# Performance work log

Measured on AMD Instinct MI355X. Metric: run time of the kernel, lower is better.

Reference implementation:

```python
import jax, jax.numpy as jnp
import numpy as np

N_NODES = 25000
N_EDGES = 400000
HIDDEN = 256
NUM_FILTERS = 256
NUM_GAUSSIANS = 50
CUTOFF = 10.0


def ssp(x):
    # ShiftedSoftplus: softplus(x) - log(2)
    return jax.nn.softplus(x) - jnp.log(2.0).astype(x.dtype)


def setup_inputs() -> dict:
    key = jax.random.key(0)
    ks = jax.random.split(key, 12)
    s = 0.05
    return {
        "h": jax.random.normal(ks[0], (N_NODES, HIDDEN), dtype=jnp.float32),
        "pos": jax.random.uniform(ks[1], (N_NODES, 3), dtype=jnp.float32) * CUTOFF,
        "lin1_w": jax.random.normal(ks[2], (HIDDEN, NUM_FILTERS), dtype=jnp.float32) * s,
        "lin2_w": jax.random.normal(ks[3], (NUM_FILTERS, HIDDEN), dtype=jnp.float32) * s,
        "lin2_b": jnp.zeros((HIDDEN,), dtype=jnp.float32),
        "mlp_w1": jax.random.normal(ks[4], (NUM_GAUSSIANS, NUM_FILTERS), dtype=jnp.float32) * s,
        "mlp_b1": jnp.zeros((NUM_FILTERS,), dtype=jnp.float32),
        "mlp_w2": jax.random.normal(ks[5], (NUM_FILTERS, NUM_FILTERS), dtype=jnp.float32) * s,
        "mlp_b2": jnp.zeros((NUM_FILTERS,), dtype=jnp.float32),
        "lin_w": jax.random.normal(ks[6], (HIDDEN, HIDDEN), dtype=jnp.float32) * s,
        "lin_b": jnp.zeros((HIDDEN,), dtype=jnp.float32),
        "edge_index": jax.random.randint(ks[7], (2, N_EDGES), 0, N_NODES, dtype=jnp.int32),
    }


def reference(h, pos, lin1_w, lin2_w, lin2_b, mlp_w1, mlp_b1, mlp_w2, mlp_b2,
              lin_w, lin_b, edge_index):
    row, col = edge_index[0], edge_index[1]  # source, target (PyG convention)

    # edge distances
    diff = pos[row] - pos[col]                       # [E, 3]
    edge_weight = jnp.linalg.norm(diff, axis=-1)     # [E]

    # GaussianSmearing(0, cutoff, num_gaussians)
    offset = jnp.linspace(0.0, CUTOFF, NUM_GAUSSIANS, dtype=h.dtype)
    coeff = -0.5 / (offset[1] - offset[0]) ** 2
    edge_attr = jnp.exp(coeff * (edge_weight[:, None] - offset) ** 2)  # [E, G]

    # CFConv filter network * cosine cutoff
    W = ssp(edge_attr @ mlp_w1 + mlp_b1) @ mlp_w2 + mlp_b2             # [E, F]
    C = 0.5 * (jnp.cos(edge_weight * (jnp.pi / CUTOFF)) + 1.0)         # [E]
    W = W * C[:, None]

    # gather - multiply - scatter-add
    x = h @ lin1_w                                                     # [N, F] (no bias)
    msg = x[row] * W                                                   # [E, F]
    agg = jax.ops.segment_sum(msg, col, num_segments=N_NODES)          # [N, F]

    x = agg @ lin2_w + lin2_b
    x = ssp(x)
    h_update = x @ lin_w + lin_b                                       # [N, H]
    return (h_update, pos)
```

## Files before the change

kernel.cpp:

```cpp
#include <hip/hip_runtime.h>
#include <hip/hip_bf16.h>

#define N_NODES 25000
#define N_EDGES 400000
#define NTILES (N_EDGES / 32)

typedef __attribute__((ext_vector_type(8))) __bf16 bf16x8;
typedef __attribute__((ext_vector_type(4))) float f32x4;
typedef __attribute__((ext_vector_type(2))) unsigned uint32x2;

#define BAR() do {                                          \
    asm volatile("s_waitcnt lgkmcnt(0)" ::: "memory");      \
    __builtin_amdgcn_s_barrier();                           \
    asm volatile("" ::: "memory");                          \
} while (0)

static __device__ __forceinline__ unsigned short bfbits(float f) {
    __bf16 h = (__bf16)f;
    return __builtin_bit_cast(unsigned short, h);
}
static __device__ __forceinline__ float bf2f(unsigned short u) {
    return __builtin_bit_cast(float, ((unsigned)u) << 16);
}
static __device__ __forceinline__ float ssp_f(float x) {
    const float t = __builtin_amdgcn_exp2f(x * 1.44269504f);
    return 0.69314718f * (__builtin_amdgcn_logf(1.f + t) - 1.f);
}

template<int EPI, int OBF, int ABF>
__global__ __launch_bounds__(256, 2)
void node_gemm(const void* __restrict__ Av, const float* __restrict__ B,
               const float* __restrict__ bias, void* __restrict__ outv, int M)
{
    extern __shared__ char lds[];
    const int tid  = threadIdx.x;
    const int half = blockIdx.x & 1;
    const int jblk = half << 7;
    const int row0 = (blockIdx.x >> 1) << 7;

    {
        const int j   = tid & 127;
        const int k2b = (tid >> 7) << 6;
        for (int i = 0; i < 64; ++i) {
            const int k = (k2b + i) * 2;
            const float b0 = B[k * 256 + jblk + j];
            const float b1 = B[(k + 1) * 256 + jblk + j];
            const unsigned pack = (unsigned)bfbits(b0) | ((unsigned)bfbits(b1) << 16);
            *(unsigned*)(lds + ((j * 512 + k * 2) ^ ((j & 7) << 4))) = pack;
        }
    }
    __syncthreads();

    const int wave = tid >> 6;
    const int l    = tid & 63;
    const int lrow = l & 15;
    const int kg   = (l >> 4) << 3;

    f32x4 acc[8][2];
    const f32x4 z4 = {0.f, 0.f, 0.f, 0.f};
    #pragma unroll
    for (int m = 0; m < 8; ++m) { acc[m][0] = z4; acc[m][1] = z4; }

    #pragma unroll
    for (int ks = 0; ks < 8; ++ks) {
        const int k0 = (ks << 5) + kg;
        bf16x8 bfr[2];
        #pragma unroll
        for (int n = 0; n < 2; ++n) {
            const int jl = (wave << 5) + (n << 4) + lrow;
            bfr[n] = *(const bf16x8*)(lds + ((jl * 512 + k0 * 2) ^ ((jl & 7) << 4)));
        }
        #pragma unroll
        for (int m = 0; m < 8; ++m) {
            const int row = row0 + (m << 4) + lrow;
            bf16x8 af;
            if (row < M) {
                if (ABF) {
                    af = *(const bf16x8*)((const __bf16*)Av + row * 256 + k0);
                } else {
                    const float* ap = (const float*)Av + row * 256 + k0;
                    const f32x4 a0 = *(const f32x4*)(ap);
                    const f32x4 a1 = *(const f32x4*)(ap + 4);
                    #pragma unroll
                    for (int b = 0; b < 4; ++b) { af[b] = (__bf16)a0[b]; af[b + 4] = (__bf16)a1[b]; }
                }
            } else {
                #pragma unroll
                for (int b = 0; b < 8; ++b) af[b] = (__bf16)0.f;
            }
            acc[m][0] = __builtin_amdgcn_mfma_f32_16x16x32_bf16(af, bfr[0], acc[m][0], 0, 0, 0);
            acc[m][1] = __builtin_amdgcn_mfma_f32_16x16x32_bf16(af, bfr[1], acc[m][1], 0, 0, 0);
        }
    }

    #pragma unroll
    for (int m = 0; m < 8; ++m) {
        #pragma unroll
        for (int n = 0; n < 2; ++n) {
            const int j = jblk + (wave << 5) + (n << 4) + lrow;
            float bv = 0.f;
            if (EPI) bv = bias[j];
            #pragma unroll
            for (int r = 0; r < 4; ++r) {
                const int row = row0 + (m << 4) + ((l >> 4) << 2) + r;
                if (row < M) {
                    float v = acc[m][n][r] + bv;
                    if (EPI == 1) v = ssp_f(v);
                    if (OBF) ((unsigned short*)outv)[row * 256 + j] = bfbits(v);
                    else     ((float*)outv)[row * 256 + j] = v;
                }
            }
        }
    }
}

__global__ void hist_kernel(const int* __restrict__ ei, int* __restrict__ hist)
{
    const int i = blockIdx.x * 256 + threadIdx.x;
    if (i < N_EDGES) atomicAdd(&hist[ei[N_EDGES + i]], 1);
}

__global__ void scan_kernel(int* __restrict__ hist)
{
    __shared__ int part[1024];
    const int t  = threadIdx.x;
    const int CH = (N_NODES + 1023) / 1024;
    const int lo = t * CH;
    const int hi = (lo + CH < N_NODES) ? lo + CH : N_NODES;
    int s = 0;
    for (int i = lo; i < hi; ++i) s += hist[i];
    part[t] = s;
    __syncthreads();
    for (int off = 1; off < 1024; off <<= 1) {
        const int v = part[t];
        const int u = (t >= off) ? part[t - off] : 0;
        __syncthreads();
        part[t] = v + u;
        __syncthreads();
    }
    int base = (t == 0) ? 0 : part[t - 1];
    for (int i = lo; i < hi; ++i) { const int v = hist[i]; hist[i] = base; base += v; }
}

__global__ void scatter_meta(const int* __restrict__ ei, const float* __restrict__ pos,
                             int* __restrict__ hist, float4* __restrict__ meta,
                             float* __restrict__ out_pos)
{
    const int i = blockIdx.x * 256 + threadIdx.x;
    if (i >= N_EDGES) return;
    if (i < N_NODES * 3) out_pos[i] = pos[i];
    const int r = ei[i];
    const int c = ei[N_EDGES + i];
    const float dx = pos[r * 3 + 0] - pos[c * 3 + 0];
    const float dy = pos[r * 3 + 1] - pos[c * 3 + 1];
    const float dz = pos[r * 3 + 2] - pos[c * 3 + 2];
    const float d  = __fsqrt_rn(dx * dx + dy * dy + dz * dz);
    const float C  = 0.5f * (__cosf(d * 0.31415926535f) + 1.f);
    const int p = atomicAdd(&hist[c], 1);
    float4 m;
    m.x = d; m.y = C;
    m.z = __int_as_float(r); m.w = __int_as_float(c);
    meta[p] = m;
}

__global__ __launch_bounds__(256, 2)
void edge_kernel(const float4* __restrict__ meta,
                 const float* __restrict__ w1, const float* __restrict__ b1,
                 const float* __restrict__ w2, const float* __restrict__ b2,
                 const unsigned short* __restrict__ xb, float* __restrict__ agg)
{
    extern __shared__ char lds[];
    char* w2t = lds;
    char* rb  = lds + 65536;
    int* colsm = (int*)(rb + 8192);

    const int tid   = threadIdx.x;
    const int wave  = tid >> 6;
    const int l     = tid & 63;
    const int lrow  = l & 15;
    const int g     = l >> 4;
    const int kg    = g << 3;
    const int half  = blockIdx.x & 1;
    const int jblk  = half << 7;
    const int group = blockIdx.x >> 1;

    {
        const int j   = tid & 127;
        const int k2b = (tid >> 7) << 6;
        for (int i = 0; i < 64; ++i) {
            const int k = (k2b + i) * 2;
            const float v0 = w2[k * 256 + jblk + j];
            const float v1 = w2[(k + 1) * 256 + jblk + j];
            const unsigned pack = (unsigned)bfbits(v0) | ((unsigned)bfbits(v1) << 16);
            *(unsigned*)(w2t + ((j * 512 + k * 2) ^ ((j & 7) << 4))) = pack;
        }
    }

    const float dlt    = 10.f / 49.f;
    const float coeff2 = (-0.5f / (dlt * dlt)) * 1.44269504f;
    bf16x8 w1f[4][2];
    #pragma unroll
    for (int n = 0; n < 4; ++n)
        #pragma unroll
        for (int ks = 0; ks < 2; ++ks) {
            bf16x8 v;
            #pragma unroll
            for (int b = 0; b < 8; ++b) {
                const int k = (ks << 5) + kg + b;
                const int j = (wave << 6) + (n << 4) + lrow;
                v[b] = (k < 50) ? (__bf16)w1[k * 256 + j] : (__bf16)0.f;
            }
            w1f[n][ks] = v;
        }
    float b1v[4], b2v[2];
    #pragma unroll
    for (int n = 0; n < 4; ++n) b1v[n] = b1[(wave << 6) + (n << 4) + lrow];
    #pragma unroll
    for (int n = 0; n < 2; ++n) b2v[n] = b2[jblk + (wave << 5) + (n << 4) + lrow];

    BAR();

    const f32x4 z4 = {0.f, 0.f, 0.f, 0.f};
    const int CH = (NTILES + 255) / 256;
    const int t0 = group * CH;
    int t1 = t0 + CH; if (t1 > NTILES) t1 = NTILES;

    const int ge  = tid >> 3;
    const int gkb = (tid & 7) << 3;

    int   rprev  = -1;
    float rs     = 0.f;
    int   rfirst = 1;
    float* aj    = agg + jblk + (tid & 127);

    float4 mv = meta[(t0 << 5) + (l & 31)];

    for (int t = t0; t < t1; ++t) {
        const float d  = mv.x;
        const float Cc = mv.y;
        const int   r  = __float_as_int(mv.z);
        const int   c  = __float_as_int(mv.w);

        if (t + 1 < t1) mv = meta[((t + 1) << 5) + (l & 31)];

        float xv[2][2][4];
        #pragma unroll
        for (int m = 0; m < 2; ++m)
            #pragma unroll
            for (int r4 = 0; r4 < 4; ++r4) {
                const int e  = (m << 4) + (g << 2) + r4;
                const int re = __shfl(r, e, 64);
                #pragma unroll
                for (int n = 0; n < 2; ++n) {
                    const int jloc = (wave << 5) + (n << 4) + lrow;
                    xv[m][n][r4] = bf2f(xb[re * 256 + jblk + jloc]);
                }
            }

        const float gd = __shfl(d, ge, 64);
        bf16x8 gv;
        #pragma unroll
        for (int b = 0; b < 8; ++b) {
            const int k = gkb + b;
            float gval = 0.f;
            if (k < 50) {
                const float u = gd - (float)k * dlt;
                gval = __builtin_amdgcn_exp2f(coeff2 * u * u);
            }
            gv[b] = (__bf16)gval;
        }

        BAR();
        *(bf16x8*)(rb + ((ge * 128 + (gkb << 1)) ^ ((ge & 7) << 4))) = gv;
        BAR();

        bf16x8 af[2][2];
        #pragma unroll
        for (int m = 0; m < 2; ++m) {
            const int e = (m << 4) + lrow;
            #pragma unroll
            for (int ks = 0; ks < 2; ++ks)
                af[m][ks] = *(const bf16x8*)(rb + ((e * 128 + ((ks << 5) + kg) * 2) ^ ((e & 7) << 4)));
        }
        f32x4 acc1[2][4];
        #pragma unroll
        for (int m = 0; m < 2; ++m)
            #pragma unroll
            for (int n = 0; n < 4; ++n) acc1[m][n] = z4;
        #pragma unroll
        for (int ks = 0; ks < 2; ++ks)
            #pragma unroll
            for (int m = 0; m < 2; ++m)
                #pragma unroll
                for (int n = 0; n < 4; ++n)
                    acc1[m][n] = __builtin_amdgcn_mfma_f32_16x16x32_bf16(af[m][ks], w1f[n][ks], acc1[m][n], 0, 0, 0);
        BAR();

        #pragma unroll
        for (int m = 0; m < 2; ++m)
            #pragma unroll
            for (int n = 0; n < 4; ++n)
                #pragma unroll
                for (int r4 = 0; r4 < 4; ++r4) {
                    const int e = (m << 4) + (g << 2) + r4;
                    const int k = (wave << 6) + (n << 4) + lrow;
                    const float v = ssp_f(acc1[m][n][r4] + b1v[n]);
                    *(__bf16*)(rb + ((e * 512 + k * 2) ^ ((e & 7) << 4))) = (__bf16)v;
                }
        BAR();

        f32x4 acc2[2][2];
        #pragma unroll
        for (int m = 0; m < 2; ++m) { acc2[m][0] = z4; acc2[m][1] = z4; }
        #pragma unroll
        for (int ks = 0; ks < 8; ++ks) {
            const int k0 = (ks << 5) + kg;
            bf16x8 bfr[2];
            #pragma unroll
            for (int n = 0; n < 2; ++n) {
                const int jl = (wave << 5) + (n << 4) + lrow;
                bfr[n] = *(const bf16x8*)(w2t + ((jl * 512 + k0 * 2) ^ ((jl & 7) << 4)));
            }
            #pragma unroll
            for (int m = 0; m < 2; ++m) {
                const int e = (m << 4) + lrow;
                const bf16x8 a = *(const bf16x8*)(rb + ((e * 512 + k0 * 2) ^ ((e & 7) << 4)));
                #pragma unroll
                for (int n = 0; n < 2; ++n)
                    acc2[m][n] = __builtin_amdgcn_mfma_f32_16x16x32_bf16(a, bfr[n], acc2[m][n], 0, 0, 0);
            }
        }
        BAR();

        #pragma unroll
        for (int m = 0; m < 2; ++m) {
            const int base_e = (m << 4) + (g << 2);
            #pragma unroll
            for (int n = 0; n < 2; ++n) {
                const int jloc = (wave << 5) + (n << 4) + lrow;
                float vv[4];
                #pragma unroll
                for (int r4 = 0; r4 < 4; ++r4) {
                    const int e  = base_e + r4;
                    const float Ce = __shfl(Cc, e, 64);
                    vv[r4] = (acc2[m][n][r4] + b2v[n]) * Ce * xv[m][n][r4];
                }
                uint32x2 pk;
                pk[0] = (unsigned)bfbits(vv[0]) | ((unsigned)bfbits(vv[1]) << 16);
                pk[1] = (unsigned)bfbits(vv[2]) | ((unsigned)bfbits(vv[3]) << 16);
                *(uint32x2*)(rb + ((jloc * 64 + (base_e << 1)) ^ ((jloc & 7) << 4))) = pk;
            }
        }
        if (tid < 32) colsm[tid] = c;
        BAR();

        if (tid < 128) {
            const int j = tid;
            const bf16x8 q0 = *(const bf16x8*)(rb + ((j * 64 +  0) ^ ((j & 7) << 4)));
            const bf16x8 q1 = *(const bf16x8*)(rb + ((j * 64 + 16) ^ ((j & 7) << 4)));
            const bf16x8 q2 = *(const bf16x8*)(rb + ((j * 64 + 32) ^ ((j & 7) << 4)));
            const bf16x8 q3 = *(const bf16x8*)(rb + ((j * 64 + 48) ^ ((j & 7) << 4)));
            #pragma unroll
            for (int e = 0; e < 32; ++e) {
                const float v = (float)(e < 8 ? q0[e] : e < 16 ? q1[e - 8] :
                                        e < 24 ? q2[e - 16] : q3[e - 24]);
                const int ce = colsm[e];
                if (ce != rprev) {
                    if (rprev >= 0) {
                        if (rfirst) { atomicAdd(aj + rprev * 256, rs); rfirst = 0; }
                        else        { aj[rprev * 256] = rs; }
                    }
                    rs = 0.f; rprev = ce;
                }
                rs += v;
            }
        }
    }
    if (tid < 128 && rprev >= 0) atomicAdd(aj + rprev * 256, rs);
}

extern "C" void kernel_launch(void* const* d_in, const int* in_sizes, int n_in,
                              void* d_out, int out_size, void* d_ws, size_t ws_size,
                              hipStream_t stream)
{
    const float* h      = (const float*)d_in[0];
    const float* pos    = (const float*)d_in[1];
    const float* lin1_w = (const float*)d_in[2];
    const float* lin2_w = (const float*)d_in[3];
    const float* lin2_b = (const float*)d_in[4];
    const float* mlp_w1 = (const float*)d_in[5];
    const float* mlp_b1 = (const float*)d_in[6];
    const float* mlp_w2 = (const float*)d_in[7];
    const float* mlp_b2 = (const float*)d_in[8];
    const float* lin_w  = (const float*)d_in[9];
    const float* lin_b  = (const float*)d_in[10];
    const int*   ei     = (const int*)d_in[11];
    float* out = (float*)d_out;

    unsigned short* xb  = (unsigned short*)d_ws;
    float*  agg  = (float*)((char*)d_ws + 12800000);
    float4* meta = (float4*)((char*)d_ws + 38400000);
    int*    hist = (int*)((char*)d_ws + 44800000);

    (void)hipFuncSetAttribute((const void*)edge_kernel,
                              hipFuncAttributeMaxDynamicSharedMemorySize, 81920);
    (void)hipFuncSetAttribute((const void*)node_gemm<0, 1, 0>,
                              hipFuncAttributeMaxDynamicSharedMemorySize, 65536);
    (void)hipFuncSetAttribute((const void*)node_gemm<1, 1, 0>,
                              hipFuncAttributeMaxDynamicSharedMemorySize, 65536);
    (void)hipFuncSetAttribute((const void*)node_gemm<2, 0, 1>,
                              hipFuncAttributeMaxDynamicSharedMemorySize, 65536);

    (void)hipMemsetAsync(agg, 0, (size_t)N_NODES * 256 * sizeof(float), stream);
    (void)hipMemsetAsync(hist, 0, (size_t)N_NODES * sizeof(int), stream);

    const dim3 blk(256);
    const int mt = (N_NODES + 127) / 128;
    const int eb = (N_EDGES + 255) / 256;

    node_gemm<0, 1, 0><<<dim3(mt * 2), blk, 65536, stream>>>(h, lin1_w, nullptr, xb, N_NODES);

    hist_kernel<<<dim3(eb), blk, 0, stream>>>(ei, hist);
    scan_kernel<<<dim3(1), dim3(1024), 0, stream>>>(hist);
    scatter_meta<<<dim3(eb), blk, 0, stream>>>(ei, pos, hist, meta, out + N_NODES * 256);

    edge_kernel<<<dim3(512), blk, 81920, stream>>>(meta, mlp_w1, mlp_b1,
                                                   mlp_w2, mlp_b2, xb, agg);

    node_gemm<1, 1, 0><<<dim3(mt * 2), blk, 65536, stream>>>(agg, lin2_w, lin2_b, xb, N_NODES);
    node_gemm<2, 0, 1><<<dim3(mt * 2), blk, 65536, stream>>>(xb, lin_w, lin_b, out, N_NODES);
}
```

Before: 449.0 us.

## Split fused edge kernel into separate filter-MLP stages with bf16 intermediate

Splits the single fused edge kernel into two kernels. The first computes the Gaussian smearing, the first filter GEMM and the shifted softplus, and writes a bf16 [E,256] intermediate to workspace. The second reads that intermediate, runs the second GEMM over a 64-column quarter of the filters per block, and does the gather-multiply-segmented scatter-add. The split is meant to relieve register and LDS pressure and raise occupancy, at the cost of an extra ~200MB round trip through HBM. It is only taken when the workspace is large enough.

Result: slower. 655.4 us (+46.0%).

```diff
diff --git a/kernel.cpp b/kernel.cpp
--- a/kernel.cpp
+++ b/kernel.cpp
@@ -164,6 +164,248 @@
 }
 
 __global__ __launch_bounds__(256, 2)
+void edge_gemm1(const float4* __restrict__ meta,
+                const float* __restrict__ w1, const float* __restrict__ b1,
+                unsigned short* __restrict__ tg)
+{
+    __shared__ char gs[8192];
+    __shared__ char tb[32768];
+
+    const int tid  = threadIdx.x;
+    const int wave = tid >> 6;
+    const int l    = tid & 63;
+    const int lrow = l & 15;
+    const int g    = l >> 4;
+    const int kg   = g << 3;
+    const int e0   = blockIdx.x << 6;
+
+    const float dlt    = 10.f / 49.f;
+    const float coeff2 = (-0.5f / (dlt * dlt)) * 1.44269504f;
+
+    bf16x8 w1f[4][2];
+    #pragma unroll
+    for (int n = 0; n < 4; ++n)
+        #pragma unroll
+        for (int ks = 0; ks < 2; ++ks) {
+            bf16x8 v;
+            #pragma unroll
+            for (int b = 0; b < 8; ++b) {
+                const int k = (ks << 5) + kg + b;
+                const int j = (wave << 6) + (n << 4) + lrow;
+                v[b] = (k < 50) ? (__bf16)w1[k * 256 + j] : (__bf16)0.f;
+            }
+            w1f[n][ks] = v;
+        }
+    float b1v[4];
+    #pragma unroll
+    for (int n = 0; n < 4; ++n) b1v[n] = b1[(wave << 6) + (n << 4) + lrow];
+
+    #pragma unroll
+    for (int s = 0; s < 2; ++s) {
+        const int slot = tid + (s << 8);
+        const int ge   = slot >> 3;
+        const int kb   = (slot & 7) << 3;
+        const float gd = meta[e0 + ge].x;
+        bf16x8 gv;
+        #pragma unroll
+        for (int b = 0; b < 8; ++b) {
+            const int k = kb + b;
+            float gval = 0.f;
+            if (k < 50) {
+                const float u = gd - (float)k * dlt;
+                gval = __builtin_amdgcn_exp2f(coeff2 * u * u);
+            }
+            gv[b] = (__bf16)gval;
+        }
+        *(bf16x8*)(gs + ((ge * 128 + (kb << 1)) ^ ((ge & 7) << 4))) = gv;
+    }
+    __syncthreads();
+
+    f32x4 acc[4][4];
+    const f32x4 z4 = {0.f, 0.f, 0.f, 0.f};
+    #pragma unroll
+    for (int m = 0; m < 4; ++m)
+        #pragma unroll
+        for (int n = 0; n < 4; ++n) acc[m][n] = z4;
+    #pragma unroll
+    for (int ks = 0; ks < 2; ++ks) {
+        #pragma unroll
+        for (int m = 0; m < 4; ++m) {
+            const int e = (m << 4) + lrow;
+            const bf16x8 af = *(const bf16x8*)(gs + ((e * 128 + (((ks << 5) + kg) << 1)) ^ ((e & 7) << 4)));
+            #pragma unroll
+            for (int n = 0; n < 4; ++n)
+                acc[m][n] = __builtin_amdgcn_mfma_f32_16x16x32_bf16(af, w1f[n][ks], acc[m][n], 0, 0, 0);
+        }
+    }
+
+    #pragma unroll
+    for (int m = 0; m < 4; ++m)
+        #pragma unroll
+        for (int n = 0; n < 4; ++n)
+            #pragma unroll
+            for (int r4 = 0; r4 < 4; ++r4) {
+                const int e = (m << 4) + (g << 2) + r4;
+                const int k = (wave << 6) + (n << 4) + lrow;
+                const float v = ssp_f(acc[m][n][r4] + b1v[n]);
+                *(__bf16*)(tb + ((e * 512 + k * 2) ^ ((e & 7) << 4))) = (__bf16)v;
+            }
+    __syncthreads();
+
+    char* dst = (char*)tg + (size_t)e0 * 512;
+    #pragma unroll
+    for (int i = 0; i < 8; ++i) {
+        const int lin = tid * 128 + i * 16;
+        const int e   = lin >> 9;
+        const int kb  = lin & 511;
+        const f32x4 v = *(const f32x4*)(tb + ((e * 512 + kb) ^ ((e & 7) << 4)));
+        *(f32x4*)(dst + lin) = v;
+    }
+}
+
+__global__ __launch_bounds__(256, 3)
+void edge_gemm2(const float4* __restrict__ meta,
+                const unsigned short* __restrict__ tg,
+                const float* __restrict__ w2, const float* __restrict__ b2,
+                const unsigned short* __restrict__ xb, float* __restrict__ agg)
+{
+    __shared__ char w2t[32768];
+    __shared__ char tb[16384];
+    __shared__ char ms[4096];
+    __shared__ int colsm[32];
+
+    const int tid  = threadIdx.x;
+    const int wave = tid >> 6;
+    const int l    = tid & 63;
+    const int lrow = l & 15;
+    const int g    = l >> 4;
+    const int kg   = g << 3;
+
+    const int chunk = blockIdx.x & 255;
+    const int q     = blockIdx.x >> 8;
+    const int jq    = q << 6;
+
+    {
+        const int j  = tid & 63;
+        const int kq = (tid >> 6) << 6;
+        for (int i = 0; i < 32; ++i) {
+            const int k = kq + i * 2;
+            const float v0 = w2[k * 256 + jq + j];
+            const float v1 = w2[(k + 1) * 256 + jq + j];
+            const unsigned pack = (unsigned)bfbits(v0) | ((unsigned)bfbits(v1) << 16);
+            *(unsigned*)(w2t + ((j * 512 + k * 2) ^ ((j & 7) << 4))) = pack;
+        }
+    }
+    const float b2v = b2[jq + (wave << 4) + lrow];
+    __syncthreads();
+
+    const int CH = 49;
+    const int t0 = chunk * CH;
+    int t1 = t0 + CH; if (t1 > NTILES) t1 = NTILES;
+
+    int   rprev  = -1;
+    float rs     = 0.f;
+    int   rfirst = 1;
+    float* aj    = agg + jq + (tid & 63);
+
+    const f32x4 z4 = {0.f, 0.f, 0.f, 0.f};
+
+    f32x4 tpre[4];
+    #pragma unroll
+    for (int i = 0; i < 4; ++i)
+        tpre[i] = *(const f32x4*)((const char*)tg + (size_t)t0 * 16384 + tid * 64 + i * 16);
+    float4 mv = meta[(t0 << 5) + (l & 31)];
+
+    for (int t = t0; t < t1; ++t) {
+        #pragma unroll
+        for (int i = 0; i < 4; ++i) {
+            const int lin = tid * 64 + i * 16;
+            const int e   = lin >> 9;
+            const int kb  = lin & 511;
+            *(f32x4*)(tb + ((e * 512 + kb) ^ ((e & 7) << 4))) = tpre[i];
+        }
+        if (tid < 32) colsm[tid] = __float_as_int(mv.w);
+        const float Cc = mv.y;
+        const int   r  = __float_as_int(mv.z);
+
+        float xvv[2][4];
+        #pragma unroll
+        for (int m = 0; m < 2; ++m)
+            #pragma unroll
+            for (int r4 = 0; r4 < 4; ++r4) {
+                const int e  = (m << 4) + (g << 2) + r4;
+                const int re = __shfl(r, e, 64);
+                xvv[m][r4] = bf2f(xb[re * 256 + jq + (wave << 4) + lrow]);
+            }
+
+        if (t + 1 < t1) {
+            mv = meta[((t + 1) << 5) + (l & 31)];
+            #pragma unroll
+            for (int i = 0; i < 4; ++i)
+                tpre[i] = *(const f32x4*)((const char*)tg + (size_t)(t + 1) * 16384 + tid * 64 + i * 16);
+        }
+
+        BAR();
+
+        f32x4 acc2[2] = {z4, z4};
+        #pragma unroll
+        for (int ks = 0; ks < 8; ++ks) {
+            const int k0 = (ks << 5) + kg;
+            const int jl = (wave << 4) + lrow;
+            const bf16x8 bfr = *(const bf16x8*)(w2t + ((jl * 512 + k0 * 2) ^ ((jl & 7) << 4)));
+            #pragma unroll
+            for (int m = 0; m < 2; ++m) {
+                const int e = (m << 4) + lrow;
+                const bf16x8 a = *(const bf16x8*)(tb + ((e * 512 + k0 * 2) ^ ((e & 7) << 4)));
+                acc2[m] = __builtin_amdgcn_mfma_f32_16x16x32_bf16(a, bfr, acc2[m], 0, 0, 0);
+            }
+        }
+
+        #pragma unroll
+        for (int m = 0; m < 2; ++m) {
+            const int base_e = (m << 4) + (g << 2);
+            const int jloc   = (wave << 4) + lrow;
+            float vv[4];
+            #pragma unroll
+            for (int r4 = 0; r4 < 4; ++r4) {
+                const int e  = base_e + r4;
+                const float Ce = __shfl(Cc, e, 64);
+                vv[r4] = (acc2[m][r4] + b2v) * Ce * xvv[m][r4];
+            }
+            uint32x2 pk;
+            pk[0] = (unsigned)bfbits(vv[0]) | ((unsigned)bfbits(vv[1]) << 16);
+            pk[1] = (unsigned)bfbits(vv[2]) | ((unsigned)bfbits(vv[3]) << 16);
+            *(uint32x2*)(ms + ((jloc * 64 + (base_e << 1)) ^ ((jloc & 7) << 4))) = pk;
+        }
+
+        BAR();
+
+        if (tid < 64) {
+            const int j = tid;
+            const bf16x8 q0 = *(const bf16x8*)(ms + ((j * 64 +  0) ^ ((j & 7) << 4)));
+            const bf16x8 q1 = *(const bf16x8*)(ms + ((j * 64 + 16) ^ ((j & 7) << 4)));
+            const bf16x8 q2 = *(const bf16x8*)(ms + ((j * 64 + 32) ^ ((j & 7) << 4)));
+            const bf16x8 q3 = *(const bf16x8*)(ms + ((j * 64 + 48) ^ ((j & 7) << 4)));
+            #pragma unroll
+            for (int e = 0; e < 32; ++e) {
+                const float v = (float)(e < 8 ? q0[e] : e < 16 ? q1[e - 8] :
+                                        e < 24 ? q2[e - 16] : q3[e - 24]);
+                const int ce = colsm[e];
+                if (ce != rprev) {
+                    if (rprev >= 0) {
+                        if (rfirst) { atomicAdd(aj + rprev * 256, rs); rfirst = 0; }
+                        else        { aj[rprev * 256] = rs; }
+                    }
+                    rs = 0.f; rprev = ce;
+                }
+                rs += v;
+            }
+        }
+    }
+    if (tid < 64 && rprev >= 0) atomicAdd(aj + rprev * 256, rs);
+}
+
+__global__ __launch_bounds__(256, 2)
 void edge_kernel(const float4* __restrict__ meta,
                  const float* __restrict__ w1, const float* __restrict__ b1,
                  const float* __restrict__ w2, const float* __restrict__ b2,
@@ -240,7 +482,6 @@
         const float Cc = mv.y;
         const int   r  = __float_as_int(mv.z);
         const int   c  = __float_as_int(mv.w);
-
         if (t + 1 < t1) mv = meta[((t + 1) << 5) + (l & 31)];
 
         float xv[2][2][4];
@@ -401,6 +642,8 @@
     float*  agg  = (float*)((char*)d_ws + 12800000);
     float4* meta = (float4*)((char*)d_ws + 38400000);
     int*    hist = (int*)((char*)d_ws + 44800000);
+    unsigned short* tg = (unsigned short*)((char*)d_ws + 44900000);
+    const bool use_split = (ws_size >= 249700000ULL);
 
     (void)hipFuncSetAttribute((const void*)edge_kernel,
                               hipFuncAttributeMaxDynamicSharedMemorySize, 81920);
@@ -424,8 +667,13 @@
     scan_kernel<<<dim3(1), dim3(1024), 0, stream>>>(hist);
     scatter_meta<<<dim3(eb), blk, 0, stream>>>(ei, pos, hist, meta, out + N_NODES * 256);
 
-    edge_kernel<<<dim3(512), blk, 81920, stream>>>(meta, mlp_w1, mlp_b1,
-                                                   mlp_w2, mlp_b2, xb, agg);
+    if (use_split) {
+        edge_gemm1<<<dim3(N_EDGES / 64), blk, 0, stream>>>(meta, mlp_w1, mlp_b1, tg);
+        edge_gemm2<<<dim3(1024), blk, 0, stream>>>(meta, tg, mlp_w2, mlp_b2, xb, agg);
+    } else {
+        edge_kernel<<<dim3(512), blk, 81920, stream>>>(meta, mlp_w1, mlp_b1,
+                                                       mlp_w2, mlp_b2, xb, agg);
+    }
 
     node_gemm<1, 1, 0><<<dim3(mt * 2), blk, 65536, stream>>>(agg, lin2_w, lin2_b, xb, N_NODES);
     node_gemm<2, 0, 1><<<dim3(mt * 2), blk, 65536, stream>>>(xb, lin_w, lin_b, out, N_NODES);
```
